# Kernel optimization log

Hardware: AMD Instinct MI355X
Metric: run time of the kernel (lower is better)

Reference implementation:

```python
import jax, jax.numpy as jnp
import numpy as np

C = 128        # in_channels
N = 80000      # nodes per type (user, item)
E = 1000000    # edges per relation
L = 400000     # link labels


def _evolve_gcn(x_src, edge_index, n_dst, p, W0, Wih, Whh, bih, bhh):
    """EvolveGCNH layer: TopK pooling -> 1-step GRU weight evolution -> GCN."""
    # TopK pooling: score = x @ p / ||p||, keep top C nodes, gate by tanh(score)
    score = x_src @ p / (jnp.linalg.norm(p) + 1e-16)          # [N_src]
    top_vals, top_idx = jax.lax.top_k(score, x_src.shape[1])   # k = C
    X_tilde = x_src[top_idx] * jnp.tanh(top_vals)[:, None]     # [C, C]
    # One GRU step: 'batch' dim = C rows of X_tilde, hidden = current weight W0
    gi = X_tilde @ Wih.T + bih                                 # [C, 3C]
    gh = W0 @ Whh.T + bhh                                      # [C, 3C]
    i_r, i_z, i_n = jnp.split(gi, 3, axis=1)
    h_r, h_z, h_n = jnp.split(gh, 3, axis=1)
    r = jax.nn.sigmoid(i_r + h_r)
    z = jax.nn.sigmoid(i_z + h_z)
    n = jnp.tanh(i_n + r * h_n)
    W = (1.0 - z) * n + z * W0                                 # evolved weight [C, C]
    # GCN propagation with symmetric degree norm, no self loops
    xw = x_src @ W                                             # [N_src, C]
    row, col = edge_index[0], edge_index[1]
    ones = jnp.ones(row.shape[0], dtype=xw.dtype)
    deg_src = jax.ops.segment_sum(ones, row, num_segments=x_src.shape[0])
    deg_dst = jax.ops.segment_sum(ones, col, num_segments=n_dst)
    inv_s = jnp.where(deg_src > 0, jax.lax.rsqrt(jnp.maximum(deg_src, 1.0)), 0.0)
    inv_d = jnp.where(deg_dst > 0, jax.lax.rsqrt(jnp.maximum(deg_dst, 1.0)), 0.0)
    norm = inv_s[row] * inv_d[col]                             # [E]
    return jax.ops.segment_sum(xw[row] * norm[:, None], col, num_segments=n_dst)


def setup_inputs() -> dict:
    key = jax.random.key(0)
    ks = jax.random.split(key, 20)
    f = lambda i, shape, s: jax.random.normal(ks[i], shape, dtype=jnp.float32) * s
    s_w = 1.0 / np.sqrt(C)
    return {
        "x_user": f(0, (N, C), 1.0),
        "x_item": f(1, (N, C), 1.0),
        "edge_ui": jax.random.randint(ks[2], (2, E), 0, N),
        "edge_iu": jax.random.randint(ks[3], (2, E), 0, N),
        "edge_label_index": jax.random.randint(ks[4], (2, L), 0, N),
        "p_ui": f(5, (C,), s_w),
        "W0_ui": f(6, (C, C), s_w),
        "Wih_ui": f(7, (3 * C, C), s_w),
        "Whh_ui": f(8, (3 * C, C), s_w),
        "bih_ui": f(9, (3 * C,), s_w),
        "bhh_ui": f(10, (3 * C,), s_w),
        "p_iu": f(11, (C,), s_w),
        "W0_iu": f(12, (C, C), s_w),
        "Wih_iu": f(13, (3 * C, C), s_w),
        "Whh_iu": f(14, (3 * C, C), s_w),
        "bih_iu": f(15, (3 * C,), s_w),
        "bhh_iu": f(16, (3 * C,), s_w),
        "W_post": f(17, (C, 2), s_w),
        "b_post": f(18, (2,), s_w),
    }


def reference(x_user, x_item, edge_ui, edge_iu, edge_label_index,
              p_ui, W0_ui, Wih_ui, Whh_ui, bih_ui, bhh_ui,
              p_iu, W0_iu, Wih_iu, Whh_iu, bih_iu, bhh_iu,
              W_post, b_post):
    # HeteroConv: one EvolveGCNH per relation, outputs grouped by dst node type
    h_item = jax.nn.relu(_evolve_gcn(x_user, edge_ui, x_item.shape[0],
                                     p_ui, W0_ui, Wih_ui, Whh_ui, bih_ui, bhh_ui))
    h_user = jax.nn.relu(_evolve_gcn(x_item, edge_iu, x_user.shape[0],
                                     p_iu, W0_iu, Wih_iu, Whh_iu, bih_iu, bhh_iu))
    # Link scorer: gather endpoints, hadamard, linear(C->2), sum over last dim
    h_src = h_user[edge_label_index[0]]                        # [L, C]
    h_dst = h_item[edge_label_index[1]]                        # [L, C]
    h = (h_src * h_dst) @ W_post + b_post                      # [L, 2]
    return jnp.sum(h, axis=-1)                                 # [L]
```

## Files before the change

### kernel.cpp

```cpp
#include <hip/hip_runtime.h>
#include <hip/hip_fp16.h>

constexpr int KC    = 128;
constexpr int NBLK  = 2048;
constexpr int CAPA  = 1024;
constexpr int CBITS = 10;
constexpr int CSZ   = 1 << CBITS;
constexpr int NBCM  = 192;

using half8   = __attribute__((ext_vector_type(8))) _Float16;
using float4v = __attribute__((ext_vector_type(4))) float;

__device__ __forceinline__ unsigned fkey(float s) {
  unsigned u = __float_as_uint(s);
  return (u & 0x80000000u) ? ~u : (u | 0x80000000u);
}

__global__ __launch_bounds__(256) void m1_cnt_scores(
    const int* __restrict__ eui, const int* __restrict__ eiu,
    unsigned* __restrict__ cnts,
    const float* __restrict__ xu, const float* __restrict__ xi,
    const float* __restrict__ pu, const float* __restrict__ pi,
    float* __restrict__ scores, unsigned* __restrict__ hist,
    __half* __restrict__ x16,
    int E, int N, int NBC, int chunk, int NTOT) {
  __shared__ unsigned hD[4 * NBCM], hS[4 * NBCM];
  int t = threadIdx.x;
  if (blockIdx.x < NBLK) {
    int blk = blockIdx.x, w = t >> 6;
    for (int b = t; b < 4 * NBCM; b += 256) { hD[b] = 0; hS[b] = 0; }
    __syncthreads();
    int lo = blk * chunk, hi = min(2 * E, lo + chunk);
    for (int i = lo + t; i < hi; i += 256) {
      int rel = i >= E;
      const int* e = rel ? eiu : eui;
      int j = i - rel * E;
      atomicAdd(&hD[w * NBCM + ((rel * N + e[E + j]) >> CBITS)], 1u);
      atomicAdd(&hS[w * NBCM + ((rel * N + e[j]) >> CBITS)], 1u);
    }
    __syncthreads();
    for (int b = t; b < NBC; b += 256) {
      cnts[(size_t)blk * NBC + b] =
          hD[b] + hD[NBCM + b] + hD[2 * NBCM + b] + hD[3 * NBCM + b];
      cnts[(size_t)NTOT + (size_t)blk * NBC + b] =
          hS[b] + hS[NBCM + b] + hS[2 * NBCM + b] + hS[3 * NBCM + b];
    }
  } else {
    int gw = (blockIdx.x - NBLK) * 8 + (t >> 5);
    if (gw >= 2 * N) return;
    int lane = t & 31;
    int rel = gw >= N;
    int r = gw - rel * N;
    const float* x = rel ? xi : xu;
    const float* p = rel ? pi : pu;
    float4 xv = ((const float4*)(x + (size_t)r * KC))[lane];
    float4 pv = ((const float4*)p)[lane];
    __half2 h0 = __floats2half2_rn(xv.x, xv.y);
    __half2 h1 = __floats2half2_rn(xv.z, xv.w);
    uint2 u; u.x = *(unsigned*)&h0; u.y = *(unsigned*)&h1;
    ((uint2*)(x16 + (size_t)gw * KC))[lane] = u;
    float s = xv.x * pv.x + xv.y * pv.y + xv.z * pv.z + xv.w * pv.w;
#pragma unroll
    for (int off = 16; off; off >>= 1) s += __shfl_down(s, off, 32);
    if (lane == 0) {
      scores[gw] = s;
      atomicAdd(&hist[rel * 65536 + (fkey(s) >> 16)], 1u);
    }
  }
}

__global__ __launch_bounds__(1024) void m2_thresh_scan1(
    const unsigned* __restrict__ cnts, unsigned* __restrict__ sc,
    unsigned* __restrict__ bsum, const unsigned* __restrict__ hist,
    unsigned* __restrict__ ctrl, int NTOT, int NBC, int SCB) {
  __shared__ __align__(16) unsigned smem[1024 + 64 + 2];
  int t = threadIdx.x;
  if (blockIdx.x < 2) {
    const unsigned* h = hist + blockIdx.x * 65536;
    unsigned* c = ctrl + blockIdx.x * 8;
    unsigned* csum = smem;
    unsigned* bs = smem + 1024;
    unsigned s = 0;
    int hi = 65536 - 64 * t;
    for (int b = hi - 64; b < hi; ++b) s += h[b];
    csum[t] = s;
    __syncthreads();
    for (int off = 1; off < 1024; off <<= 1) {
      unsigned add = (t >= off) ? csum[t - off] : 0;
      __syncthreads();
      csum[t] += add;
      __syncthreads();
    }
    unsigned above = (t == 0) ? 0u : csum[t - 1];
    if (csum[t] >= 128u && above < 128u) { smem[1088] = (unsigned)t; smem[1089] = above; }
    __syncthreads();
    int chi = 65536 - 64 * (int)smem[1088];
    unsigned s_above = smem[1089];
    if (t < 64) bs[t] = h[chi - 1 - t];
    __syncthreads();
    if (t < 64) {
      unsigned v = bs[t], cum = v;
#pragma unroll
      for (int off = 1; off < 64; off <<= 1) {
        unsigned u = __shfl_up(cum, off, 64);
        if (t >= off) cum += u;
      }
      unsigned prev = cum - v;
      if (s_above + cum >= 128u && s_above + prev < 128u)
        c[0] = (unsigned)(chi - 1 - t);
    }
  } else {
    unsigned* wsum = smem;
    int vb = blockIdx.x - 2;
    int seg = vb / SCB, lb = vb % SCB;
    int li = lb * 1024 + t;
    unsigned v = 0;
    if (li < NTOT) {
      int b = li >> 11, blk = li & (NBLK - 1);
      v = cnts[(size_t)seg * NTOT + (size_t)blk * NBC + b];
    }
    unsigned inc = v;
#pragma unroll
    for (int off = 1; off < 64; off <<= 1) {
      unsigned u = __shfl_up(inc, off, 64);
      if ((t & 63) >= off) inc += u;
    }
    int w = t >> 6;
    if ((t & 63) == 63) wsum[w] = inc;
    __syncthreads();
    unsigned wbase = 0;
#pragma unroll
    for (int j = 0; j < 16; ++j) if (j < w) wbase += wsum[j];
    if (li < NTOT) sc[(size_t)seg * NTOT + li] = wbase + inc - v;
    if (t == 1023) bsum[vb] = wbase + inc;
  }
}

__global__ __launch_bounds__(512) void m3_scan2_compact(
    unsigned* __restrict__ bsum, int nb,
    const float* __restrict__ scores, unsigned* __restrict__ ctrl,
    int* __restrict__ cand_idx, float* __restrict__ cand_val, int N) {
  __shared__ unsigned wsum[8];
  if (blockIdx.x < 2) {
    unsigned* bs = bsum + blockIdx.x * nb;
    int t = threadIdx.x;
    unsigned v = (t < nb) ? bs[t] : 0;
    unsigned inc = v;
#pragma unroll
    for (int off = 1; off < 64; off <<= 1) {
      unsigned u = __shfl_up(inc, off, 64);
      if ((t & 63) >= off) inc += u;
    }
    int w = t >> 6;
    if ((t & 63) == 63) wsum[w] = inc;
    __syncthreads();
    unsigned wbase = 0;
#pragma unroll
    for (int j = 0; j < 8; ++j) if (j < w) wbase += wsum[j];
    if (t < nb) bs[t] = wbase + inc - v;
  } else {
    int i = (blockIdx.x - 2) * 512 + threadIdx.x;
    if (i >= 2 * N) return;
    int rel = i >= N;
    float s = scores[i];
    if ((fkey(s) >> 16) >= ctrl[rel * 8]) {
      unsigned pos = atomicAdd(&ctrl[rel * 8 + 1], 1u);
      if (pos < 2048u) {
        cand_idx[rel * 2048 + pos] = i - rel * N;
        cand_val[rel * 2048 + pos] = s;
      }
    }
  }
}

__global__ __launch_bounds__(256) void m4_topk_part(
    const int* __restrict__ eui, const int* __restrict__ eiu,
    const unsigned* __restrict__ cnts, const unsigned* __restrict__ sc,
    const unsigned* __restrict__ bsum,
    unsigned* __restrict__ recsD, unsigned short* __restrict__ recsS,
    const unsigned* __restrict__ ctrl,
    const int* __restrict__ cand_idx, const float* __restrict__ cand_val,
    const float* __restrict__ pu, const float* __restrict__ pi,
    int* __restrict__ top_idx, float* __restrict__ top_tanh,
    int E, int N, int NBC, int chunk, int NTOT, int SCB) {
  __shared__ __align__(16) char smem[16896];
  int t = threadIdx.x;
  if (blockIdx.x < 2) {
    float* vals = (float*)smem;
    int*   idxs = (int*)(smem + 8192);
    float* red  = (float*)(smem + 16384);
    int rel = blockIdx.x;
    const float* p = rel ? pi : pu;
    int n = (int)ctrl[rel * 8 + 1]; if (n > 2048) n = 2048;
    for (int i = t; i < n; i += 256) {
      vals[i] = cand_val[rel * 2048 + i];
      idxs[i] = cand_idx[rel * 2048 + i];
    }
    if (t < 128) { float pv = p[t]; red[t] = pv * pv; }
    __syncthreads();
    for (int off = 64; off; off >>= 1) {
      if (t < off) red[t] += red[t + off];
      __syncthreads();
    }
    float pn = sqrtf(red[0]) + 1e-16f;
    for (int c = t; c < n; c += 256) {
      float v = vals[c]; int id = idxs[c];
      int rank = 0;
      for (int j = 0; j < n; ++j) {
        float vj = vals[j];
        rank += (vj > v) || (vj == v && idxs[j] < id);
      }
      if (rank < KC) {
        top_idx[rel * KC + rank] = id;
        top_tanh[rel * KC + rank] = tanhf(v / pn);
      }
    }
  } else {
    unsigned* wsumD  = (unsigned*)smem;
    unsigned* wsumS  = (unsigned*)(smem + 64);
    unsigned* curD   = (unsigned*)(smem + 1024);
    unsigned* curS   = (unsigned*)(smem + 2048);
    unsigned* deltaD = (unsigned*)(smem + 3072);
    unsigned* deltaS = (unsigned*)(smem + 4096);
    unsigned* stageD = (unsigned*)(smem + 5120);
    unsigned short* stageS = (unsigned short*)(smem + 9216);
    unsigned char* bktD = (unsigned char*)(smem + 11264);
    unsigned char* bktS = (unsigned char*)(smem + 12288);
    int blk = blockIdx.x - 2;
    int lane = t & 63, w = t >> 6;
    unsigned vD = (t < NBC) ? cnts[(size_t)blk * NBC + t] : 0;
    unsigned vS = (t < NBC) ? cnts[(size_t)NTOT + (size_t)blk * NBC + t] : 0;
    unsigned incD = vD, incS = vS;
#pragma unroll
    for (int off = 1; off < 64; off <<= 1) {
      unsigned uD = __shfl_up(incD, off, 64);
      unsigned uS = __shfl_up(incS, off, 64);
      if (lane >= off) { incD += uD; incS += uS; }
    }
    if (lane == 63) { wsumD[w] = incD; wsumS[w] = incS; }
    __syncthreads();
    unsigned wbD = 0, wbS = 0;
#pragma unroll
    for (int j = 0; j < 4; ++j) if (j < w) { wbD += wsumD[j]; wbS += wsumS[j]; }
    if (t < NBC) {
      unsigned excD = wbD + incD - vD;
      curD[t] = excD;
      int li = t * NBLK + blk;
      deltaD[t] = sc[li] + bsum[li >> 10] - excD;
      unsigned excS = wbS + incS - vS;
      curS[t] = excS;
      deltaS[t] = sc[NTOT + li] + bsum[SCB + (li >> 10)] - excS;
    }
    __syncthreads();
    int lo = blk * chunk, hi = min(2 * E, lo + chunk);
    for (int i = lo + t; i < hi; i += 256) {
      int rel = i >= E;
      const int* e = rel ? eiu : eui;
      int j = i - rel * E;
      int src_g = rel * N + e[j];
      int dst_g = rel * N + e[E + j];
      int bD = dst_g >> CBITS;
      unsigned pD = atomicAdd(&curD[bD], 1u);
      stageD[pD] = (unsigned)src_g | ((unsigned)(dst_g & (CSZ - 1)) << 18);
      bktD[pD] = (unsigned char)bD;
      int bS = src_g >> CBITS;
      unsigned pS = atomicAdd(&curS[bS], 1u);
      stageS[pS] = (unsigned short)(src_g & (CSZ - 1));
      bktS[pS] = (unsigned char)bS;
    }
    __syncthreads();
    int cnt = hi - lo;
    for (int j = t; j < cnt; j += 256) {
      recsD[deltaD[bktD[j]] + j] = stageD[j];
      recsS[deltaS[bktS[j]] + j] = stageS[j];
    }
  }
}

__global__ __launch_bounds__(1024) void m5_refine_gru(
    const unsigned* __restrict__ sc, const unsigned* __restrict__ bsum,
    const unsigned* __restrict__ recsD, const unsigned short* __restrict__ recsS,
    int* __restrict__ ssrc, int* __restrict__ deg_dst, int* __restrict__ endp,
    int* __restrict__ deg_src,
    const float* __restrict__ xu, const float* __restrict__ xi,
    const int* __restrict__ top_idx, const float* __restrict__ top_tanh,
    const float* __restrict__ W0u, const float* __restrict__ W0i,
    const float* __restrict__ Wihu, const float* __restrict__ Wihi,
    const float* __restrict__ Whhu, const float* __restrict__ Whhi,
    const float* __restrict__ bihu, const float* __restrict__ bihi,
    const float* __restrict__ bhhu, const float* __restrict__ bhhi,
    __half* __restrict__ Wt,
    int E, int NBC, int N2, int NTOT, int SCB) {
  __shared__ __align__(16) char smem[8256];
  int t = threadIdx.x;
  if ((int)blockIdx.x < NBC) {
    unsigned* hist = (unsigned*)smem;
    unsigned* cur  = (unsigned*)(smem + 4096);
    unsigned* t16  = (unsigned*)(smem + 8192);
    int c = blockIdx.x;
    int liLo = c * NBLK;
    int lo = (int)(sc[liLo] + bsum[liLo >> 10]);
    int hi;
    if (c + 1 < NBC) {
      int liHi = (c + 1) * NBLK;
      hi = (int)(sc[liHi] + bsum[liHi >> 10]);
    } else hi = 2 * E;
    hist[t] = 0;
    __syncthreads();
    for (int j = lo + t; j < hi; j += 1024)
      atomicAdd(&hist[recsD[j] >> 18], 1u);
    __syncthreads();
    unsigned v = hist[t];
    unsigned inc = v;
#pragma unroll
    for (int off = 1; off < 64; off <<= 1) {
      unsigned u = __shfl_up(inc, off, 64);
      if ((t & 63) >= off) inc += u;
    }
    int w = t >> 6;
    if ((t & 63) == 63) t16[w] = inc;
    __syncthreads();
    unsigned wbase = 0;
    for (int j = 0; j < 16; ++j) if (j < w) wbase += t16[j];
    unsigned exc = wbase + inc - v;
    cur[t] = exc;
    int node = c * CSZ + t;
    if (node < N2) {
      deg_dst[node] = (int)v;
      endp[node] = lo + (int)(exc + v);
    }
    __syncthreads();
    for (int j = lo + t; j < hi; j += 1024) {
      unsigned rec = recsD[j];
      unsigned pos = atomicAdd(&cur[rec >> 18], 1u);
      ssrc[lo + (int)pos] = (int)((rec & 0x3FFFFu) << 8);
    }
  } else if ((int)blockIdx.x < 2 * NBC) {
    unsigned* hist = (unsigned*)smem;
    int c = blockIdx.x - NBC;
    int liLo = c * NBLK;
    int lo = (int)(sc[NTOT + liLo] + bsum[SCB + (liLo >> 10)]);
    int hi;
    if (c + 1 < NBC) {
      int liHi = (c + 1) * NBLK;
      hi = (int)(sc[NTOT + liHi] + bsum[SCB + (liHi >> 10)]);
    } else hi = 2 * E;
    hist[t] = 0;
    __syncthreads();
    for (int j = lo + t; j < hi; j += 1024)
      atomicAdd(&hist[(unsigned)recsS[j]], 1u);
    __syncthreads();
    int node = c * CSZ + t;
    if (node < N2) deg_src[node] = (int)hist[t];
  } else {
    int gb = blockIdx.x - 2 * NBC;
    int rel = gb >> 7, c = gb & 127;
    const float* x   = rel ? xi   : xu;
    const float* W0  = rel ? W0i  : W0u;
    const float* Wih = rel ? Wihi : Wihu;
    const float* Whh = rel ? Whhi : Whhu;
    const float* bih = rel ? bihi : bihu;
    const float* bhh = rel ? bhhi : bhhu;
    float* xt = (float*)smem;
    float* w0 = (float*)(smem + 512);
    if (t < KC) {
      xt[t] = x[(size_t)top_idx[rel * KC + c] * KC + t] * top_tanh[rel * KC + c];
      w0[t] = W0[c * KC + t];
    }
    __syncthreads();
    if (t >= KC) return;
    int k = t;
    float gir = bih[k], giz = bih[KC + k], gin = bih[2 * KC + k];
    float ghr = bhh[k], ghz = bhh[KC + k], ghn = bhh[2 * KC + k];
    const float* wr = Wih + (size_t)k * KC;
    const float* wz = Wih + (size_t)(KC + k) * KC;
    const float* wn = Wih + (size_t)(2 * KC + k) * KC;
    const float* vr = Whh + (size_t)k * KC;
    const float* vz = Whh + (size_t)(KC + k) * KC;
    const float* vn = Whh + (size_t)(2 * KC + k) * KC;
    for (int j = 0; j < KC; ++j) {
      float xj = xt[j], hj = w0[j];
      gir += xj * wr[j]; giz += xj * wz[j]; gin += xj * wn[j];
      ghr += hj * vr[j]; ghz += hj * vz[j]; ghn += hj * vn[j];
    }
    float r = 1.f / (1.f + expf(-(gir + ghr)));
    float z = 1.f / (1.f + expf(-(giz + ghz)));
    float nn = tanhf(gin + r * ghn);
    float w = (1.f - z) * nn + z * w0[k];
    Wt[(size_t)rel * KC * KC + (size_t)k * KC + c] = __float2half_rn(w);
  }
}

__global__ __launch_bounds__(256) void k_gemm(const __half* __restrict__ x16,
                                              const __half* __restrict__ Wt,
                                              const int* __restrict__ deg_src,
                                              __half* __restrict__ xw, int N) {
  __shared__ __half Ws[KC * KC];
  __shared__ __half outs[64 * 136];
  int rel = (blockIdx.x * 64) >= N;
  int t = threadIdx.x;
  const uint4* wg = (const uint4*)(Wt + (size_t)rel * KC * KC);
#pragma unroll
  for (int i = 0; i < 8; ++i)
    ((uint4*)Ws)[t + 256 * i] = wg[t + 256 * i];
  __syncthreads();
  int wid = t >> 6, lane = t & 63;
  int l15 = lane & 15, quad = lane >> 4;
  int row0 = blockIdx.x * 64 + wid * 16;
  half8 a[4];
  const __half* xrow = x16 + (size_t)(row0 + l15) * KC + quad * 8;
#pragma unroll
  for (int ks = 0; ks < 4; ++ks) a[ks] = *(const half8*)(xrow + ks * 32);
  float4v acc[8];
#pragma unroll
  for (int nt = 0; nt < 8; ++nt) {
    acc[nt] = (float4v){0.f, 0.f, 0.f, 0.f};
#pragma unroll
    for (int ks = 0; ks < 4; ++ks) {
      half8 b = *(const half8*)&Ws[(nt * 16 + l15) * KC + ks * 32 + quad * 8];
      acc[nt] = __builtin_amdgcn_mfma_f32_16x16x32_f16(a[ks], b, acc[nt], 0, 0, 0);
    }
  }
  float scv[4];
#pragma unroll
  for (int r = 0; r < 4; ++r) {
    int dg = deg_src[row0 + quad * 4 + r];
    scv[r] = dg > 0 ? rsqrtf((float)dg) : 0.f;
  }
  __half* ob = outs + (size_t)wid * 16 * 136;
#pragma unroll
  for (int nt = 0; nt < 8; ++nt)
#pragma unroll
    for (int r = 0; r < 4; ++r)
      ob[(quad * 4 + r) * 136 + nt * 16 + l15] = __float2half_rn(acc[nt][r] * scv[r]);
  __syncthreads();
  size_t gbase = (size_t)blockIdx.x * 64 * KC;
#pragma unroll
  for (int i = 0; i < 4; ++i) {
    int idx = t + 256 * i;
    int rr = idx >> 4, cc = idx & 15;
    *(uint4*)(xw + gbase + (size_t)rr * KC + cc * 8) =
        *(const uint4*)(outs + (size_t)rr * 136 + cc * 8);
  }
}

__global__ void k_agg(const __half* __restrict__ xw, const int* __restrict__ ssrc,
                      const int* __restrict__ endp, const int* __restrict__ deg_dst,
                      __half* __restrict__ h, int n2) {
  int gw = (int)((blockIdx.x * blockDim.x + threadIdx.x) >> 6);
  if (gw >= n2) return;
  int lane = threadIdx.x & 63;
  int q = lane >> 4, l16 = lane & 15;
  int d = deg_dst[gw];
  int end = endp[gw], start = end - d;
  const char* xb = (const char*)xw;
  __half2 z = __floats2half2_rn(0.f, 0.f);
  __half2 a0[4], a1[4], a2[4], a3[4];
#pragma unroll
  for (int k = 0; k < 4; ++k) { a0[k] = z; a1[k] = z; a2[k] = z; a3[k] = z; }
  for (int i = start + q; i < end; i += 16) {
    int i1 = i + 4, i2 = i + 8, i3 = i + 12;
    bool b1 = i1 < end, b2 = i2 < end, b3 = i3 < end;
    int r0 = ssrc[i], r1, r2, r3;
    if (b1) r1 = ssrc[i1];
    if (b2) r2 = ssrc[i2];
    if (b3) r3 = ssrc[i3];
    uint4 u0 = *(const uint4*)(xb + r0 + l16 * 16);
    uint4 u1, u2, u3;
    if (b1) u1 = *(const uint4*)(xb + r1 + l16 * 16);
    if (b2) u2 = *(const uint4*)(xb + r2 + l16 * 16);
    if (b3) u3 = *(const uint4*)(xb + r3 + l16 * 16);
    {
      const __half2* p = (const __half2*)&u0;
#pragma unroll
      for (int k = 0; k < 4; ++k) a0[k] = __hadd2(a0[k], p[k]);
    }
    if (b1) {
      const __half2* p = (const __half2*)&u1;
#pragma unroll
      for (int k = 0; k < 4; ++k) a1[k] = __hadd2(a1[k], p[k]);
    }
    if (b2) {
      const __half2* p = (const __half2*)&u2;
#pragma unroll
      for (int k = 0; k < 4; ++k) a2[k] = __hadd2(a2[k], p[k]);
    }
    if (b3) {
      const __half2* p = (const __half2*)&u3;
#pragma unroll
      for (int k = 0; k < 4; ++k) a3[k] = __hadd2(a3[k], p[k]);
    }
  }
  float f[8];
#pragma unroll
  for (int k = 0; k < 4; ++k) {
    float2 x0 = __half22float2(a0[k]);
    float2 x1 = __half22float2(a1[k]);
    float2 x2 = __half22float2(a2[k]);
    float2 x3 = __half22float2(a3[k]);
    f[2 * k]     = (x0.x + x1.x) + (x2.x + x3.x);
    f[2 * k + 1] = (x0.y + x1.y) + (x2.y + x3.y);
  }
#pragma unroll
  for (int k = 0; k < 8; ++k) {
    f[k] += __shfl_xor(f[k], 16, 64);
    f[k] += __shfl_xor(f[k], 32, 64);
  }
  if (q == 0) {
    float invd = d > 0 ? rsqrtf((float)d) : 0.f;
    __half2 pk[4];
#pragma unroll
    for (int k = 0; k < 4; ++k)
      pk[k] = __floats2half2_rn(fmaxf(f[2 * k] * invd, 0.f),
                                fmaxf(f[2 * k + 1] * invd, 0.f));
    uint4 u;
    u.x = *(unsigned*)&pk[0]; u.y = *(unsigned*)&pk[1];
    u.z = *(unsigned*)&pk[2]; u.w = *(unsigned*)&pk[3];
    ((uint4*)(h + (size_t)gw * KC))[l16] = u;
  }
}

__global__ void k_links(const __half* __restrict__ h,
                        const int* __restrict__ srcs, const int* __restrict__ dsts,
                        const float* __restrict__ Wp, const float* __restrict__ bp,
                        float* __restrict__ out, int L, int N) {
  int tid = blockIdx.x * blockDim.x + threadIdx.x;
  int lane = threadIdx.x & 63;
  int q = lane >> 4, l16 = lane & 15;
  int gq = (tid >> 6) * 4 + q;
  int nq = (int)((gridDim.x * blockDim.x) >> 6) * 4;
  float w8[8];
#pragma unroll
  for (int k = 0; k < 4; ++k) {
    float4 w = ((const float4*)Wp)[l16 * 4 + k];
    w8[2 * k] = w.x + w.y; w8[2 * k + 1] = w.z + w.w;
  }
  float bs = bp[0] + bp[1];
  const __half* hu = h + (size_t)N * KC;
  for (int li = gq; li < L; li += nq) {
    int s = srcs[li], dd = dsts[li];
    uint4 ua = ((const uint4*)(hu + (size_t)s * KC))[l16];
    uint4 ub = ((const uint4*)(h + (size_t)dd * KC))[l16];
    const __half2* pa = (const __half2*)&ua;
    const __half2* pb = (const __half2*)&ub;
    float acc = 0.f;
#pragma unroll
    for (int k = 0; k < 4; ++k) {
      float2 fa = __half22float2(pa[k]);
      float2 fb = __half22float2(pb[k]);
      acc += fa.x * fb.x * w8[2 * k] + fa.y * fb.y * w8[2 * k + 1];
    }
#pragma unroll
    for (int off = 8; off; off >>= 1) acc += __shfl_xor(acc, off, 64);
    if (l16 == 0) out[li] = acc + bs;
  }
}

extern "C" void kernel_launch(void* const* d_in, const int* in_sizes, int n_in,
                              void* d_out, int out_size, void* d_ws, size_t ws_size,
                              hipStream_t stream) {
  const float* x_user = (const float*)d_in[0];
  const float* x_item = (const float*)d_in[1];
  const int*   edge_ui = (const int*)d_in[2];
  const int*   edge_iu = (const int*)d_in[3];
  const int*   elab    = (const int*)d_in[4];
  const float* p_ui   = (const float*)d_in[5];
  const float* W0_ui  = (const float*)d_in[6];
  const float* Wih_ui = (const float*)d_in[7];
  const float* Whh_ui = (const float*)d_in[8];
  const float* bih_ui = (const float*)d_in[9];
  const float* bhh_ui = (const float*)d_in[10];
  const float* p_iu   = (const float*)d_in[11];
  const float* W0_iu  = (const float*)d_in[12];
  const float* Wih_iu = (const float*)d_in[13];
  const float* Whh_iu = (const float*)d_in[14];
  const float* bih_iu = (const float*)d_in[15];
  const float* bhh_iu = (const float*)d_in[16];
  const float* W_post = (const float*)d_in[17];
  const float* b_post = (const float*)d_in[18];
  const int N = in_sizes[0] / KC;
  const int E = in_sizes[2] / 2;
  const int L = in_sizes[4] / 2;
  const int N2 = 2 * N;
  const int NBC = (N2 + CSZ - 1) >> CBITS;
  const int chunk = (2 * E + NBLK - 1) / NBLK;
  const int NTOT = NBC * NBLK;
  const int SCB = (NTOT + 1023) / 1024;

  char* wsp = (char*)d_ws;
  auto carve = [&](size_t bytes) -> void* {
    void* p = (void*)wsp;
    wsp += (bytes + 255) & ~(size_t)255;
    return p;
  };
  const size_t histB = 2 * 65536 * 4;
  const size_t zBytes = histB + 256;
  char*     zbase    = (char*)carve(zBytes);
  unsigned* hist     = (unsigned*)zbase;
  unsigned* ctrl     = (unsigned*)(zbase + histB);
  int*      deg_src  = (int*)carve((size_t)N2 * 4);
  __half*   x16      = (__half*)carve((size_t)N2 * KC * 2);
  __half*   xw       = (__half*)carve((size_t)N2 * KC * 2);
  __half*   h        = (__half*)carve((size_t)N2 * KC * 2);
  float*    scores   = (float*)carve((size_t)N2 * 4);
  int*      cand_idx = (int*)carve(2 * 2048 * 4);
  float*    cand_val = (float*)carve(2 * 2048 * 4);
  int*      top_idx  = (int*)carve(2 * KC * 4);
  float*    top_tanh = (float*)carve(2 * KC * 4);
  __half*   Wt16     = (__half*)carve(2 * KC * KC * 2);
  unsigned* cnts     = (unsigned*)carve((size_t)2 * NTOT * 4);
  unsigned* sc       = (unsigned*)carve((size_t)2 * NTOT * 4);
  unsigned* bsum     = (unsigned*)carve((size_t)2 * SCB * 4);
  unsigned* recsD    = (unsigned*)carve((size_t)2 * E * 4);
  unsigned short* recsS = (unsigned short*)carve((size_t)2 * E * 2);
  int*      ssrc     = (int*)carve((size_t)2 * E * 4);
  int*      deg_dst  = (int*)carve((size_t)N2 * 4);
  int*      endp     = (int*)carve((size_t)N2 * 4);

  hipMemsetAsync(zbase, 0, zBytes, stream);

  const int SBLK = (N2 + 7) / 8;
  m1_cnt_scores<<<NBLK + SBLK, 256, 0, stream>>>(edge_ui, edge_iu, cnts,
                                                 x_user, x_item, p_ui, p_iu,
                                                 scores, hist, x16,
                                                 E, N, NBC, chunk, NTOT);
  m2_thresh_scan1<<<2 + 2 * SCB, 1024, 0, stream>>>(cnts, sc, bsum, hist, ctrl,
                                                    NTOT, NBC, SCB);
  m3_scan2_compact<<<2 + (N2 + 511) / 512, 512, 0, stream>>>(bsum, SCB, scores, ctrl,
                                                             cand_idx, cand_val, N);
  m4_topk_part<<<2 + NBLK, 256, 0, stream>>>(edge_ui, edge_iu, cnts, sc, bsum,
                                             recsD, recsS, ctrl, cand_idx, cand_val,
                                             p_ui, p_iu, top_idx, top_tanh,
                                             E, N, NBC, chunk, NTOT, SCB);
  m5_refine_gru<<<2 * NBC + 2 * KC, 1024, 0, stream>>>(sc, bsum, recsD, recsS, ssrc,
                                                       deg_dst, endp, deg_src,
                                                       x_user, x_item, top_idx, top_tanh,
                                                       W0_ui, W0_iu, Wih_ui, Wih_iu,
                                                       Whh_ui, Whh_iu, bih_ui, bih_iu,
                                                       bhh_ui, bhh_iu, Wt16,
                                                       E, NBC, N2, NTOT, SCB);
  k_gemm<<<N2 / 64, 256, 0, stream>>>(x16, Wt16, deg_src, xw, N);
  k_agg<<<(N2 + 3) / 4, 256, 0, stream>>>(xw, ssrc, endp, deg_dst, h, N2);
  k_links<<<2048, 256, 0, stream>>>(h, elab, elab + L, W_post, b_post,
                                    (float*)d_out, L, N);
}
```

Measured before the change: 396.2 us.

## Merge threshold, scan and compaction kernels; recompute block-sum scan per block

Removes one kernel launch by folding the second-level scan of block sums into the consumers: each partition and refine block now rescans the small bsum array in shared memory with a single wave. The top-k threshold search moves into the compaction blocks, so each compaction block recomputes the histogram threshold redundantly, and the threshold and compaction work now share one launch with the first-level scan. This trades a launch boundary and global round-trip for redundant per-block work, including reading 64K histogram bins in every compaction block.

```diff
diff --git a/kernel.cpp b/kernel.cpp
--- a/kernel.cpp
+++ b/kernel.cpp
@@ -14,6 +14,65 @@
 __device__ __forceinline__ unsigned fkey(float s) {
   unsigned u = __float_as_uint(s);
   return (u & 0x80000000u) ? ~u : (u | 0x80000000u);
+}
+
+__device__ __forceinline__ void wave_scan(const unsigned* __restrict__ g,
+                                          unsigned* __restrict__ out,
+                                          int n, int t) {
+  unsigned carry = 0;
+  for (int base = 0; base < n; base += 64) {
+    int idx = base + t;
+    unsigned v = (idx < n) ? g[idx] : 0;
+    unsigned inc = v;
+#pragma unroll
+    for (int off = 1; off < 64; off <<= 1) {
+      unsigned u = __shfl_up(inc, off, 64);
+      if (t >= off) inc += u;
+    }
+    if (idx < n) out[idx] = carry + inc - v;
+    carry += __shfl(inc, 63, 64);
+  }
+}
+
+__device__ unsigned find_thresh(const unsigned* __restrict__ h, unsigned* smem) {
+  int t = threadIdx.x;
+  unsigned* wsum = smem + 1024;
+  unsigned s = 0;
+  int hi = 65536 - 64 * t;
+  for (int b = hi - 64; b < hi; ++b) s += h[b];
+  unsigned inc = s;
+#pragma unroll
+  for (int off = 1; off < 64; off <<= 1) {
+    unsigned u = __shfl_up(inc, off, 64);
+    if ((t & 63) >= off) inc += u;
+  }
+  int w = t >> 6;
+  if ((t & 63) == 63) wsum[w] = inc;
+  __syncthreads();
+  unsigned wb = 0;
+#pragma unroll
+  for (int j = 0; j < 16; ++j) if (j < w) wb += wsum[j];
+  unsigned cum = wb + inc, above = cum - s;
+  if (cum >= 128u && above < 128u) { wsum[16] = (unsigned)t; wsum[17] = above; }
+  __syncthreads();
+  int chunk = (int)wsum[16];
+  unsigned s_above = wsum[17];
+  int chi = 65536 - 64 * chunk;
+  if (t < 64) {
+    unsigned v = h[chi - 1 - t], cum2 = v;
+#pragma unroll
+    for (int off = 1; off < 64; off <<= 1) {
+      unsigned u = __shfl_up(cum2, off, 64);
+      if (t >= off) cum2 += u;
+    }
+    unsigned prev = cum2 - v;
+    if (s_above + cum2 >= 128u && s_above + prev < 128u)
+      wsum[18] = (unsigned)(chi - 1 - t);
+  }
+  __syncthreads();
+  unsigned r = wsum[18];
+  __syncthreads();
+  return r;
 }
 
 __global__ __launch_bounds__(256) void m1_cnt_scores(
@@ -69,49 +128,18 @@
   }
 }
 
-__global__ __launch_bounds__(1024) void m2_thresh_scan1(
+__global__ __launch_bounds__(1024) void m2_scan1_compact(
     const unsigned* __restrict__ cnts, unsigned* __restrict__ sc,
     unsigned* __restrict__ bsum, const unsigned* __restrict__ hist,
-    unsigned* __restrict__ ctrl, int NTOT, int NBC, int SCB) {
-  __shared__ __align__(16) unsigned smem[1024 + 64 + 2];
+    unsigned* __restrict__ ctrl,
+    const float* __restrict__ scores,
+    int* __restrict__ cand_idx, float* __restrict__ cand_val,
+    int NTOT, int NBC, int SCB, int N) {
+  __shared__ __align__(16) unsigned smem[1024 + 32];
   int t = threadIdx.x;
-  if (blockIdx.x < 2) {
-    const unsigned* h = hist + blockIdx.x * 65536;
-    unsigned* c = ctrl + blockIdx.x * 8;
-    unsigned* csum = smem;
-    unsigned* bs = smem + 1024;
-    unsigned s = 0;
-    int hi = 65536 - 64 * t;
-    for (int b = hi - 64; b < hi; ++b) s += h[b];
-    csum[t] = s;
-    __syncthreads();
-    for (int off = 1; off < 1024; off <<= 1) {
-      unsigned add = (t >= off) ? csum[t - off] : 0;
-      __syncthreads();
-      csum[t] += add;
-      __syncthreads();
-    }
-    unsigned above = (t == 0) ? 0u : csum[t - 1];
-    if (csum[t] >= 128u && above < 128u) { smem[1088] = (unsigned)t; smem[1089] = above; }
-    __syncthreads();
-    int chi = 65536 - 64 * (int)smem[1088];
-    unsigned s_above = smem[1089];
-    if (t < 64) bs[t] = h[chi - 1 - t];
-    __syncthreads();
-    if (t < 64) {
-      unsigned v = bs[t], cum = v;
-#pragma unroll
-      for (int off = 1; off < 64; off <<= 1) {
-        unsigned u = __shfl_up(cum, off, 64);
-        if (t >= off) cum += u;
-      }
-      unsigned prev = cum - v;
-      if (s_above + cum >= 128u && s_above + prev < 128u)
-        c[0] = (unsigned)(chi - 1 - t);
-    }
-  } else {
+  if ((int)blockIdx.x < 2 * SCB) {
     unsigned* wsum = smem;
-    int vb = blockIdx.x - 2;
+    int vb = blockIdx.x;
     int seg = vb / SCB, lb = vb % SCB;
     int li = lb * 1024 + t;
     unsigned v = 0;
@@ -133,47 +161,30 @@
     for (int j = 0; j < 16; ++j) if (j < w) wbase += wsum[j];
     if (li < NTOT) sc[(size_t)seg * NTOT + li] = wbase + inc - v;
     if (t == 1023) bsum[vb] = wbase + inc;
-  }
-}
-
-__global__ __launch_bounds__(512) void m3_scan2_compact(
-    unsigned* __restrict__ bsum, int nb,
-    const float* __restrict__ scores, unsigned* __restrict__ ctrl,
-    int* __restrict__ cand_idx, float* __restrict__ cand_val, int N) {
-  __shared__ unsigned wsum[8];
-  if (blockIdx.x < 2) {
-    unsigned* bs = bsum + blockIdx.x * nb;
-    int t = threadIdx.x;
-    unsigned v = (t < nb) ? bs[t] : 0;
-    unsigned inc = v;
-#pragma unroll
-    for (int off = 1; off < 64; off <<= 1) {
-      unsigned u = __shfl_up(inc, off, 64);
-      if ((t & 63) >= off) inc += u;
-    }
-    int w = t >> 6;
-    if ((t & 63) == 63) wsum[w] = inc;
-    __syncthreads();
-    unsigned wbase = 0;
-#pragma unroll
-    for (int j = 0; j < 8; ++j) if (j < w) wbase += wsum[j];
-    if (t < nb) bs[t] = wbase + inc - v;
   } else {
-    int i = (blockIdx.x - 2) * 512 + threadIdx.x;
-    if (i >= 2 * N) return;
-    int rel = i >= N;
-    float s = scores[i];
-    if ((fkey(s) >> 16) >= ctrl[rel * 8]) {
-      unsigned pos = atomicAdd(&ctrl[rel * 8 + 1], 1u);
-      if (pos < 2048u) {
-        cand_idx[rel * 2048 + pos] = i - rel * N;
-        cand_val[rel * 2048 + pos] = s;
+    int cb = blockIdx.x - 2 * SCB;
+    int i = cb * 1024 + t;
+    int r0 = (cb * 1024) >= N;
+    int r1 = (cb * 1024 + 1023) >= N;
+    unsigned thr0 = find_thresh(hist + r0 * 65536, smem);
+    unsigned thr1 = thr0;
+    if (r1 != r0) thr1 = find_thresh(hist + r1 * 65536, smem);
+    if (i < 2 * N) {
+      int rel = i >= N;
+      unsigned thr = (rel == r0) ? thr0 : thr1;
+      float s = scores[i];
+      if ((fkey(s) >> 16) >= thr) {
+        unsigned pos = atomicAdd(&ctrl[rel * 8 + 1], 1u);
+        if (pos < 2048u) {
+          cand_idx[rel * 2048 + pos] = i - rel * N;
+          cand_val[rel * 2048 + pos] = s;
+        }
       }
     }
   }
 }
 
-__global__ __launch_bounds__(256) void m4_topk_part(
+__global__ __launch_bounds__(256) void m3_topk_part(
     const int* __restrict__ eui, const int* __restrict__ eiu,
     const unsigned* __restrict__ cnts, const unsigned* __restrict__ sc,
     const unsigned* __restrict__ bsum,
@@ -216,18 +227,23 @@
       }
     }
   } else {
-    unsigned* wsumD  = (unsigned*)smem;
-    unsigned* wsumS  = (unsigned*)(smem + 64);
-    unsigned* curD   = (unsigned*)(smem + 1024);
-    unsigned* curS   = (unsigned*)(smem + 2048);
-    unsigned* deltaD = (unsigned*)(smem + 3072);
-    unsigned* deltaS = (unsigned*)(smem + 4096);
-    unsigned* stageD = (unsigned*)(smem + 5120);
-    unsigned short* stageS = (unsigned short*)(smem + 9216);
-    unsigned char* bktD = (unsigned char*)(smem + 11264);
-    unsigned char* bktS = (unsigned char*)(smem + 12288);
+    unsigned* bsD    = (unsigned*)smem;
+    unsigned* bsS    = (unsigned*)(smem + 1280);
+    unsigned* wsumD  = (unsigned*)(smem + 2560);
+    unsigned* wsumS  = (unsigned*)(smem + 2624);
+    unsigned* curD   = (unsigned*)(smem + 2688);
+    unsigned* curS   = (unsigned*)(smem + 3712);
+    unsigned* deltaD = (unsigned*)(smem + 4736);
+    unsigned* deltaS = (unsigned*)(smem + 5760);
+    unsigned* stageD = (unsigned*)(smem + 6784);
+    unsigned short* stageS = (unsigned short*)(smem + 10880);
+    unsigned char* bktD = (unsigned char*)(smem + 12928);
+    unsigned char* bktS = (unsigned char*)(smem + 13952);
     int blk = blockIdx.x - 2;
     int lane = t & 63, w = t >> 6;
+    if (w == 0) wave_scan(bsum, bsD, SCB, lane);
+    else if (w == 1) wave_scan(bsum + SCB, bsS, SCB, lane);
+    __syncthreads();
     unsigned vD = (t < NBC) ? cnts[(size_t)blk * NBC + t] : 0;
     unsigned vS = (t < NBC) ? cnts[(size_t)NTOT + (size_t)blk * NBC + t] : 0;
     unsigned incD = vD, incS = vS;
@@ -246,10 +262,10 @@
       unsigned excD = wbD + incD - vD;
       curD[t] = excD;
       int li = t * NBLK + blk;
-      deltaD[t] = sc[li] + bsum[li >> 10] - excD;
+      deltaD[t] = sc[li] + bsD[li >> 10] - excD;
       unsigned excS = wbS + incS - vS;
       curS[t] = excS;
-      deltaS[t] = sc[NTOT + li] + bsum[SCB + (li >> 10)] - excS;
+      deltaS[t] = sc[NTOT + li] + bsS[li >> 10] - excS;
     }
     __syncthreads();
     int lo = blk * chunk, hi = min(2 * E, lo + chunk);
@@ -277,7 +293,7 @@
   }
 }
 
-__global__ __launch_bounds__(1024) void m5_refine_gru(
+__global__ __launch_bounds__(1024) void m4_refine_gru(
     const unsigned* __restrict__ sc, const unsigned* __restrict__ bsum,
     const unsigned* __restrict__ recsD, const unsigned short* __restrict__ recsS,
     int* __restrict__ ssrc, int* __restrict__ deg_dst, int* __restrict__ endp,
@@ -291,22 +307,24 @@
     const float* __restrict__ bhhu, const float* __restrict__ bhhi,
     __half* __restrict__ Wt,
     int E, int NBC, int N2, int NTOT, int SCB) {
-  __shared__ __align__(16) char smem[8256];
+  __shared__ __align__(16) char smem[9600];
   int t = threadIdx.x;
   if ((int)blockIdx.x < NBC) {
     unsigned* hist = (unsigned*)smem;
     unsigned* cur  = (unsigned*)(smem + 4096);
     unsigned* t16  = (unsigned*)(smem + 8192);
+    unsigned* bs   = (unsigned*)(smem + 8256);
     int c = blockIdx.x;
+    if ((t >> 6) == 0) wave_scan(bsum, bs, SCB, t & 63);
+    hist[t] = 0;
+    __syncthreads();
     int liLo = c * NBLK;
-    int lo = (int)(sc[liLo] + bsum[liLo >> 10]);
+    int lo = (int)(sc[liLo] + bs[liLo >> 10]);
     int hi;
     if (c + 1 < NBC) {
       int liHi = (c + 1) * NBLK;
-      hi = (int)(sc[liHi] + bsum[liHi >> 10]);
+      hi = (int)(sc[liHi] + bs[liHi >> 10]);
     } else hi = 2 * E;
-    hist[t] = 0;
-    __syncthreads();
     for (int j = lo + t; j < hi; j += 1024)
       atomicAdd(&hist[recsD[j] >> 18], 1u);
     __syncthreads();
@@ -337,16 +355,18 @@
     }
   } else if ((int)blockIdx.x < 2 * NBC) {
     unsigned* hist = (unsigned*)smem;
+    unsigned* bs   = (unsigned*)(smem + 8256);
     int c = blockIdx.x - NBC;
+    if ((t >> 6) == 0) wave_scan(bsum + SCB, bs, SCB, t & 63);
+    hist[t] = 0;
+    __syncthreads();
     int liLo = c * NBLK;
-    int lo = (int)(sc[NTOT + liLo] + bsum[SCB + (liLo >> 10)]);
+    int lo = (int)(sc[NTOT + liLo] + bs[liLo >> 10]);
     int hi;
     if (c + 1 < NBC) {
       int liHi = (c + 1) * NBLK;
-      hi = (int)(sc[NTOT + liHi] + bsum[SCB + (liHi >> 10)]);
+      hi = (int)(sc[NTOT + liHi] + bs[liHi >> 10]);
     } else hi = 2 * E;
-    hist[t] = 0;
-    __syncthreads();
     for (int j = lo + t; j < hi; j += 1024)
       atomicAdd(&hist[(unsigned)recsS[j]], 1u);
     __syncthreads();
@@ -624,15 +644,15 @@
                                                  x_user, x_item, p_ui, p_iu,
                                                  scores, hist, x16,
                                                  E, N, NBC, chunk, NTOT);
-  m2_thresh_scan1<<<2 + 2 * SCB, 1024, 0, stream>>>(cnts, sc, bsum, hist, ctrl,
-                                                    NTOT, NBC, SCB);
-  m3_scan2_compact<<<2 + (N2 + 511) / 512, 512, 0, stream>>>(bsum, SCB, scores, ctrl,
-                                                             cand_idx, cand_val, N);
-  m4_topk_part<<<2 + NBLK, 256, 0, stream>>>(edge_ui, edge_iu, cnts, sc, bsum,
+  const int CPB = (N2 + 1023) / 1024;
+  m2_scan1_compact<<<2 * SCB + CPB, 1024, 0, stream>>>(cnts, sc, bsum, hist, ctrl,
+                                                       scores, cand_idx, cand_val,
+                                                       NTOT, NBC, SCB, N);
+  m3_topk_part<<<2 + NBLK, 256, 0, stream>>>(edge_ui, edge_iu, cnts, sc, bsum,
                                              recsD, recsS, ctrl, cand_idx, cand_val,
                                              p_ui, p_iu, top_idx, top_tanh,
                                              E, N, NBC, chunk, NTOT, SCB);
-  m5_refine_gru<<<2 * NBC + 2 * KC, 1024, 0, stream>>>(sc, bsum, recsD, recsS, ssrc,
+  m4_refine_gru<<<2 * NBC + 2 * KC, 1024, 0, stream>>>(sc, bsum, recsD, recsS, ssrc,
                                                        deg_dst, endp, deg_src,
                                                        x_user, x_item, top_idx, top_tanh,
                                                        W0_ui, W0_iu, Wih_ui, Wih_iu,
```

New measurement: 418.7 us. 1.06x slower.
